# Kernel tuning notes

Measured on AMD Instinct MI355X. Metric: run time of the kernel, lower is better.

Reference implementation:

```python
import jax, jax.numpy as jnp
import numpy as np

DIM = 64
HEADS = 4
EPS_LN = 1e-6
EPS_NORM = 1e-12


def _dwconv(x, w):
    # depthwise 3x3, SAME padding; x: [B,C,H,W], w: [C,1,3,3]
    return jax.lax.conv_general_dilated(
        x, w, window_strides=(1, 1), padding='SAME',
        feature_group_count=x.shape[1],
        dimension_numbers=('NCHW', 'OIHW', 'NCHW'))


def setup_inputs() -> dict:
    key = jax.random.key(0)
    ks = jax.random.split(key, 10)
    s = 0.05
    inp = {
        'x': jax.random.normal(ks[0], (8, DIM, 256, 256), dtype=jnp.float32),
        'ln_w': jnp.ones((DIM,), jnp.float32),
        'ln_b': jnp.zeros((DIM,), jnp.float32),
        'w_q': jax.random.normal(ks[1], (DIM, DIM), jnp.float32) * s,
        'w_k': jax.random.normal(ks[2], (DIM, DIM), jnp.float32) * s,
        'w_v': jax.random.normal(ks[3], (DIM, DIM), jnp.float32) * s,
        'dw_q': jax.random.normal(ks[4], (DIM, 1, 3, 3), jnp.float32) * s,
        'dw_k': jax.random.normal(ks[5], (DIM, 1, 3, 3), jnp.float32) * s,
        'dw_v': jax.random.normal(ks[6], (DIM, 1, 3, 3), jnp.float32) * s,
        'w_proj': jax.random.normal(ks[7], (DIM, DIM, 3, 3), jnp.float32) * s,
        'w_comp': jax.random.normal(ks[8], (DIM // 4, DIM), jnp.float32) * s,
        'temperature': jnp.ones((HEADS, 1, 1), jnp.float32),
    }
    return inp


def reference(x, ln_w, ln_b, w_q, w_k, w_v, dw_q, dw_k, dw_v, w_proj, w_comp, temperature):
    b, c, h, w = x.shape
    heads = temperature.shape[0]
    hd = c // heads  # per-head channels

    # LayerNorm over channel dim (per spatial location), biased variance
    mu = jnp.mean(x, axis=1, keepdims=True)
    var = jnp.mean((x - mu) ** 2, axis=1, keepdims=True)
    xn = (x - mu) / jnp.sqrt(var + EPS_LN)
    xn = xn * ln_w[None, :, None, None] + ln_b[None, :, None, None]

    # 1x1 projections then depthwise 3x3
    q = _dwconv(jnp.einsum('oc,bchw->bohw', w_q, xn), dw_q)
    k = _dwconv(jnp.einsum('oc,bchw->bohw', w_k, xn), dw_k)
    v = _dwconv(jnp.einsum('oc,bchw->bohw', w_v, xn), dw_v)

    # [b, heads, hd, h*w]
    q = q.reshape(b, heads, hd, h * w)
    k = k.reshape(b, heads, hd, h * w)
    v = v.reshape(b, heads, hd, h * w)

    # L2 normalize along spatial axis (torch F.normalize: x / max(||x||, eps))
    q = q / jnp.maximum(jnp.linalg.norm(q, axis=-1, keepdims=True), EPS_NORM)
    k = k / jnp.maximum(jnp.linalg.norm(k, axis=-1, keepdims=True), EPS_NORM)

    # channel attention: [b, heads, hd, hd]
    attn = jnp.einsum('bhcn,bhdn->bhcd', q, k) * temperature[None]
    attn = jax.nn.softmax(attn, axis=-1)
    out = jnp.einsum('bhcd,bhdn->bhcn', attn, v).reshape(b, c, h, w)

    # 3x3 projection + residual (residual is the normalized x, per source)
    out = jax.lax.conv_general_dilated(
        out, w_proj, window_strides=(1, 1), padding='SAME',
        dimension_numbers=('NCHW', 'OIHW', 'NCHW')) + xn

    # 1x1 compress to dim//4
    return jnp.einsum('oc,bchw->bohw', w_comp, out)
```

## Files before the change

### kernel.cpp

```cpp
#include <hip/hip_runtime.h>
#include <hip/hip_bf16.h>
#include <stdint.h>

#define BB 8
#define CC 64
#define HH 256
#define WW 256
#define NPIX 65536
#define HEADS 4
#define HD 16
#define PRS 76

using bf16 = __hip_bfloat16;
typedef __attribute__((ext_vector_type(8))) short short8;
typedef __attribute__((ext_vector_type(4))) float f32x4;

__device__ __forceinline__ float bf2f(bf16 v) { return __bfloat162float(v); }
__device__ __forceinline__ bf16 f2bf(float v) { return __float2bfloat16(v); }
__device__ __forceinline__ short f2bfs(float f) { bf16 h = __float2bfloat16(f); return *reinterpret_cast<short*>(&h); }
__device__ __forceinline__ float bfs2f(short s) { return __uint_as_float(((uint32_t)(uint16_t)s) << 16); }
__device__ __forceinline__ uint32_t pk2(float a, float b) {
  return (uint32_t)(uint16_t)f2bfs(a) | ((uint32_t)(uint16_t)f2bfs(b) << 16);
}
__device__ __forceinline__ short8 zero8() { short8 z = {0, 0, 0, 0, 0, 0, 0, 0}; return z; }

__device__ __forceinline__ void load8bf(const bf16* p, float* o) {
  uint4 u = *reinterpret_cast<const uint4*>(p);
  o[0] = __uint_as_float(u.x << 16);
  o[1] = __uint_as_float(u.x & 0xffff0000u);
  o[2] = __uint_as_float(u.y << 16);
  o[3] = __uint_as_float(u.y & 0xffff0000u);
  o[4] = __uint_as_float(u.z << 16);
  o[5] = __uint_as_float(u.z & 0xffff0000u);
  o[6] = __uint_as_float(u.w << 16);
  o[7] = __uint_as_float(u.w & 0xffff0000u);
}

__global__ void k_prep(const float* __restrict__ w_comp, const float* __restrict__ w_proj,
                       const float* __restrict__ w_q, const float* __restrict__ w_k,
                       const float* __restrict__ w_v,
                       short* __restrict__ wcpb, short* __restrict__ wqkvb,
                       short* __restrict__ wcb) {
  int idx = blockIdx.x * 256 + threadIdx.x;
  if (idx < 9 * 16 * 64) {
    int c = idx & 63;
    int o = (idx >> 6) & 15;
    int kk = idx >> 10;
    float acc = 0.f;
    for (int m = 0; m < 64; ++m)
      acc += w_comp[o * 64 + m] * w_proj[(m * 64 + c) * 9 + kk];
    wcpb[idx] = f2bfs(acc);
  }
  if (idx < 3 * 4096) {
    const float* Ws[3] = {w_q, w_k, w_v};
    wqkvb[idx] = f2bfs(Ws[idx >> 12][idx & 4095]);
  }
  if (idx < 1024) wcb[idx] = f2bfs(w_comp[idx]);
}

__global__ __launch_bounds__(256)
void k_ln(const float* __restrict__ x, const float* __restrict__ ln_w,
          const float* __restrict__ ln_b, short* __restrict__ xnb) {
  const int tid = threadIdx.x;
  const int b = blockIdx.x >> 8;
  const int n = ((blockIdx.x & 255) << 8) + tid;
  const float* xp = x + (size_t)b * CC * NPIX + n;
  float v[64];
  float s = 0.f, s2 = 0.f;
#pragma unroll
  for (int c = 0; c < 64; ++c) {
    float t0 = xp[(size_t)c * NPIX];
    v[c] = t0; s += t0; s2 += t0 * t0;
  }
  const float mu = s * (1.f / 64.f);
  const float r = rsqrtf(s2 * (1.f / 64.f) - mu * mu + 1e-6f);
  short* op = xnb + ((size_t)b * NPIX + n) * 64;
#pragma unroll
  for (int c8 = 0; c8 < 8; ++c8) {
    uint32_t pk[4];
#pragma unroll
    for (int j = 0; j < 4; ++j) {
      const int c0 = c8 * 8 + 2 * j;
      float f0 = (v[c0] - mu) * r * ln_w[c0] + ln_b[c0];
      float f1 = (v[c0 + 1] - mu) * r * ln_w[c0 + 1] + ln_b[c0 + 1];
      pk[j] = pk2(f0, f1);
    }
    *reinterpret_cast<uint4*>(op + c8 * 8) = make_uint4(pk[0], pk[1], pk[2], pk[3]);
  }
}

__global__ __launch_bounds__(512)
void k_qkv(const short* __restrict__ xnb, const short* __restrict__ wqkvb,
           const short* __restrict__ wcb,
           const float* __restrict__ dw_q, const float* __restrict__ dw_k,
           const float* __restrict__ dw_v,
           bf16* __restrict__ qo, bf16* __restrict__ ko,
           short* __restrict__ aov, short* __restrict__ res16) {
  __shared__ short pr_s[336 * PRS];
  const int tid = threadIdx.x;
  const int lane = tid & 63;
  const int wv = tid >> 6;
  const int olocal = lane & 15;
  const int g = lane >> 4;
  const int t = blockIdx.y;
  const int tx = blockIdx.x & 15, ty = (blockIdx.x >> 4) & 15, b = blockIdx.x >> 8;
  const int x0 = tx * 16 - 1, y0 = ty * 16 - 1;

  if (t == 0) {
    short8 wc0 = *reinterpret_cast<const short8*>(wcb + olocal * 64 + g * 8);
    short8 wc1 = *reinterpret_cast<const short8*>(wcb + olocal * 64 + 32 + g * 8);
#pragma unroll
    for (int t2 = 0; t2 < 2; ++t2) {
      const int oy = wv * 2 + t2;
      const int n = (ty * 16 + oy) * WW + tx * 16 + olocal;
      const short* bb = xnb + ((size_t)b * NPIX + n) * 64 + g * 8;
      short8 b0 = *reinterpret_cast<const short8*>(bb);
      short8 b1 = *reinterpret_cast<const short8*>(bb + 32);
      f32x4 acc = {0.f, 0.f, 0.f, 0.f};
      acc = __builtin_amdgcn_mfma_f32_16x16x32_bf16(wc0, b0, acc, 0, 0, 0);
      acc = __builtin_amdgcn_mfma_f32_16x16x32_bf16(wc1, b1, acc, 0, 0, 0);
      uint2 st;
      st.x = pk2(acc[0], acc[1]);
      st.y = pk2(acc[2], acc[3]);
      *reinterpret_cast<uint2*>(&res16[((size_t)b * NPIX + n) * 16 + g * 4]) = st;
    }
  }

  short8 Bt[4][2];
#pragma unroll
  for (int ot = 0; ot < 4; ++ot) {
    const short* wb = wqkvb + t * 4096 + (ot * 16 + olocal) * 64 + g * 8;
    Bt[ot][0] = *reinterpret_cast<const short8*>(wb);
    Bt[ot][1] = *reinterpret_cast<const short8*>(wb + 32);
  }

  short8 a0[3], a1[3];
#pragma unroll
  for (int j = 0; j < 3; ++j) {
    const int pt = wv + j * 8;
    const int p = pt * 16 + olocal;
    const int py = y0 + p / 18;
    const int px_ = x0 + p % 18;
    const bool vld = (pt < 21) && (p < 324) && ((unsigned)py < 256u) && ((unsigned)px_ < 256u);
    if (vld) {
      const short* ab = xnb + ((size_t)b * NPIX + py * WW + px_) * 64 + g * 8;
      a0[j] = *reinterpret_cast<const short8*>(ab);
      a1[j] = *reinterpret_cast<const short8*>(ab + 32);
    } else {
      a0[j] = zero8();
      a1[j] = zero8();
    }
  }
#pragma unroll
  for (int j = 0; j < 3; ++j) {
    const int pt = wv + j * 8;
    if (pt >= 21) continue;
#pragma unroll
    for (int ot = 0; ot < 4; ++ot) {
      f32x4 acc = {0.f, 0.f, 0.f, 0.f};
      acc = __builtin_amdgcn_mfma_f32_16x16x32_bf16(a0[j], Bt[ot][0], acc, 0, 0, 0);
      acc = __builtin_amdgcn_mfma_f32_16x16x32_bf16(a1[j], Bt[ot][1], acc, 0, 0, 0);
#pragma unroll
      for (int r = 0; r < 4; ++r)
        pr_s[(pt * 16 + g * 4 + r) * PRS + ot * 16 + olocal] = f2bfs(acc[r]);
    }
  }
  __syncthreads();

  const float* dmt = (t == 0) ? dw_q : (t == 1) ? dw_k : dw_v;
  float dmr[8][9];
#pragma unroll
  for (int u = 0; u < 8; ++u)
#pragma unroll
    for (int kk = 0; kk < 9; ++kk)
      dmr[u][kk] = dmt[(wv * 8 + u) * 9 + kk];
  bf16* ob = ((t == 0) ? qo : ko) + (size_t)b * CC * NPIX;
#pragma unroll
  for (int i = 0; i < 4; ++i) {
    const int pxl = lane + i * 64;
    const int oy = pxl >> 4, ox = pxl & 15;
    float acc8[8] = {0.f, 0.f, 0.f, 0.f, 0.f, 0.f, 0.f, 0.f};
#pragma unroll
    for (int ky = 0; ky < 3; ++ky)
#pragma unroll
      for (int kx = 0; kx < 3; ++kx) {
        const short8 pv = *reinterpret_cast<const short8*>(
            &pr_s[((oy + ky) * 18 + ox + kx) * PRS + wv * 8]);
        const int kk = ky * 3 + kx;
#pragma unroll
        for (int u = 0; u < 8; ++u)
          acc8[u] += dmr[u][kk] * bfs2f(pv[u]);
      }
    const int n = (ty * 16 + oy) * WW + tx * 16 + ox;
    if (t < 2) {
#pragma unroll
      for (int u = 0; u < 8; ++u)
        ob[(size_t)(wv * 8 + u) * NPIX + n] = f2bf(acc8[u]);
    } else {
      uint4 st = make_uint4(pk2(acc8[0], acc8[1]), pk2(acc8[2], acc8[3]),
                            pk2(acc8[4], acc8[5]), pk2(acc8[6], acc8[7]));
      *reinterpret_cast<uint4*>(&aov[((size_t)b * NPIX + n) * 64 + wv * 8]) = st;
    }
  }
}

__global__ __launch_bounds__(256)
void k_logits(const bf16* __restrict__ q, const bf16* __restrict__ kk_,
              float* __restrict__ Spart, float* __restrict__ Qpart,
              float* __restrict__ Kpart) {
  const int tid = threadIdx.x;
  const int lane = tid & 63;
  const int wv = tid >> 6;
  const int bh = blockIdx.x >> 6;
  const int chunk = blockIdx.x & 63;
  const int row = lane & 15;
  const int g = lane >> 4;
  const short* qp = (const short*)q + (size_t)(bh * HD + row) * NPIX;
  const short* kp = (const short*)kk_ + (size_t)(bh * HD + row) * NPIX;
  const int n0 = chunk * 1024 + wv * 256 + g * 8;
  f32x4 s = {0.f, 0.f, 0.f, 0.f};
  f32x4 sq = {0.f, 0.f, 0.f, 0.f};
  f32x4 sk = {0.f, 0.f, 0.f, 0.f};
#pragma unroll
  for (int it = 0; it < 8; ++it) {
    const int n = n0 + it * 32;
    short8 qa = *reinterpret_cast<const short8*>(qp + n);
    short8 ka = *reinterpret_cast<const short8*>(kp + n);
    s  = __builtin_amdgcn_mfma_f32_16x16x32_bf16(qa, ka, s, 0, 0, 0);
    sq = __builtin_amdgcn_mfma_f32_16x16x32_bf16(qa, qa, sq, 0, 0, 0);
    sk = __builtin_amdgcn_mfma_f32_16x16x32_bf16(ka, ka, sk, 0, 0, 0);
  }
  const size_t tile = (size_t)blockIdx.x * 4 + wv;
  float* sp = Spart + tile * 256;
#pragma unroll
  for (int r = 0; r < 4; ++r)
    sp[(g * 4 + r) * 16 + row] = s[r];
  if ((row >> 2) == g) {
    Qpart[tile * 16 + row] = sq[row & 3];
    Kpart[tile * 16 + row] = sk[row & 3];
  }
}

__global__ __launch_bounds__(256)
void k_softmax(const float* __restrict__ Spart, const float* __restrict__ Qpart,
               const float* __restrict__ Kpart, const float* __restrict__ temp,
               float* __restrict__ attn) {
  const int tid = threadIdx.x;
  const int bh = blockIdx.x;
  const int i = tid >> 4, j = tid & 15;
  float S = 0.f, qs = 0.f, ks = 0.f;
  const size_t t0 = (size_t)bh * 256;
  for (int c = 0; c < 256; ++c) {
    S += Spart[(t0 + c) * 256 + tid];
    qs += Qpart[(t0 + c) * 16 + i];
    ks += Kpart[(t0 + c) * 16 + j];
  }
  float nq = fmaxf(sqrtf(qs), 1e-12f);
  float nk = fmaxf(sqrtf(ks), 1e-12f);
  float val = S / (nq * nk) * temp[bh & 3];
  float m = val;
  for (int d = 1; d < 16; d <<= 1) m = fmaxf(m, __shfl_xor(m, d));
  float e = __expf(val - m);
  float s = e;
  for (int d = 1; d < 16; d <<= 1) s += __shfl_xor(s, d);
  attn[bh * 256 + tid] = e / s;
}

__global__ __launch_bounds__(256)
void k_attv(const float* __restrict__ attn, short* __restrict__ aov) {
  const int tid = threadIdx.x;
  const int bh = blockIdx.x >> 8;
  const int b = bh >> 2, h = bh & 3;
  const int n = ((blockIdx.x & 255) << 8) + tid;
  __shared__ float a_s[256];
  a_s[tid] = attn[bh * 256 + tid];
  __syncthreads();
  short* vp = aov + ((size_t)b * NPIX + n) * 64 + h * 16;
  float vv[16];
  load8bf((const bf16*)vp, vv);
  load8bf((const bf16*)(vp + 8), vv + 8);
  float o[16];
#pragma unroll
  for (int i = 0; i < 16; ++i) {
    float acc = 0.f;
#pragma unroll
    for (int j = 0; j < 16; ++j) acc += a_s[i * 16 + j] * vv[j];
    o[i] = acc;
  }
  uint4 lo = make_uint4(pk2(o[0], o[1]), pk2(o[2], o[3]), pk2(o[4], o[5]), pk2(o[6], o[7]));
  uint4 hi = make_uint4(pk2(o[8], o[9]), pk2(o[10], o[11]), pk2(o[12], o[13]), pk2(o[14], o[15]));
  *reinterpret_cast<uint4*>(vp) = lo;
  *reinterpret_cast<uint4*>(vp + 8) = hi;
}

__global__ __launch_bounds__(256)
void k_final(const short* __restrict__ wcpb, const short* __restrict__ ao,
             const short* __restrict__ res16, float* __restrict__ out) {
  const int tid = threadIdx.x;
  const int lane = tid & 63;
  const int wv = tid >> 6;
  const int olocal = lane & 15;
  const int g = lane >> 4;
  const int tx = blockIdx.x & 15, ty = (blockIdx.x >> 4) & 15, b = blockIdx.x >> 8;

  short8 WA[9][2];
#pragma unroll
  for (int kk = 0; kk < 9; ++kk) {
    const short* wb = wcpb + (kk * 16 + olocal) * 64 + g * 8;
    WA[kk][0] = *reinterpret_cast<const short8*>(wb);
    WA[kk][1] = *reinterpret_cast<const short8*>(wb + 32);
  }

#pragma unroll
  for (int t = 0; t < 4; ++t) {
    const int oy = wv * 4 + t;
    const int gyc = ty * 16 + oy;
    const int n0 = gyc * WW + tx * 16;
    uint2 rv = *reinterpret_cast<const uint2*>(
        &res16[((size_t)b * NPIX + n0 + olocal) * 16 + g * 4]);
    f32x4 acc;
    acc[0] = __uint_as_float(rv.x << 16);
    acc[1] = __uint_as_float(rv.x & 0xffff0000u);
    acc[2] = __uint_as_float(rv.y << 16);
    acc[3] = __uint_as_float(rv.y & 0xffff0000u);
#pragma unroll
    for (int ky = 0; ky < 3; ++ky) {
      const int gy = gyc + ky - 1;
      if ((unsigned)gy < 256u) {
#pragma unroll
        for (int kx = 0; kx < 3; ++kx) {
          const int gx = tx * 16 + kx - 1 + olocal;
          const bool vld = (unsigned)gx < 256u;
          const short* ap = ao + ((size_t)b * NPIX + gy * WW + gx) * 64 + g * 8;
          short8 b0, b1;
          if (vld) {
            b0 = *reinterpret_cast<const short8*>(ap);
            b1 = *reinterpret_cast<const short8*>(ap + 32);
          } else {
            b0 = zero8();
            b1 = zero8();
          }
          acc = __builtin_amdgcn_mfma_f32_16x16x32_bf16(WA[ky * 3 + kx][0], b0, acc, 0, 0, 0);
          acc = __builtin_amdgcn_mfma_f32_16x16x32_bf16(WA[ky * 3 + kx][1], b1, acc, 0, 0, 0);
        }
      }
    }
    float* op = out + ((size_t)b * 16 + g * 4) * NPIX + n0 + olocal;
    op[0] = acc[0];
    op[NPIX] = acc[1];
    op[2 * NPIX] = acc[2];
    op[3 * NPIX] = acc[3];
  }
}

extern "C" void kernel_launch(void* const* d_in, const int* in_sizes, int n_in,
                              void* d_out, int out_size, void* d_ws, size_t ws_size,
                              hipStream_t stream) {
  const float* x      = (const float*)d_in[0];
  const float* ln_w   = (const float*)d_in[1];
  const float* ln_b   = (const float*)d_in[2];
  const float* w_q    = (const float*)d_in[3];
  const float* w_k    = (const float*)d_in[4];
  const float* w_v    = (const float*)d_in[5];
  const float* dw_q   = (const float*)d_in[6];
  const float* dw_k   = (const float*)d_in[7];
  const float* dw_v   = (const float*)d_in[8];
  const float* w_proj = (const float*)d_in[9];
  const float* w_comp = (const float*)d_in[10];
  const float* temp   = (const float*)d_in[11];
  float* out = (float*)d_out;

  const size_t SPX = (size_t)BB * NPIX;
  short* xnb   = (short*)d_ws;
  short* qb    = xnb + SPX * 64;
  short* kb    = qb + SPX * 64;
  short* aov   = kb + SPX * 64;
  short* res16 = aov + SPX * 64;
  short* wcpb  = res16 + SPX * 16;
  short* wqkvb = wcpb + 9216;
  short* wcb   = wqkvb + 12288;
  float* Spart = (float*)(wcb + 1024);
  float* Qpart = Spart + 32 * 256 * 256;
  float* Kpart = Qpart + 32 * 256 * 16;
  float* attn  = Kpart + 32 * 256 * 16;

  k_prep<<<52, 256, 0, stream>>>(w_comp, w_proj, w_q, w_k, w_v, wcpb, wqkvb, wcb);
  k_ln<<<2048, 256, 0, stream>>>(x, ln_w, ln_b, xnb);
  dim3 gqkv(2048, 3);
  k_qkv<<<gqkv, 512, 0, stream>>>(xnb, wqkvb, wcb, dw_q, dw_k, dw_v,
                                  (bf16*)qb, (bf16*)kb, aov, res16);
  k_logits<<<2048, 256, 0, stream>>>((const bf16*)qb, (const bf16*)kb, Spart, Qpart, Kpart);
  k_softmax<<<32, 256, 0, stream>>>(Spart, Qpart, Kpart, temp, attn);
  k_attv<<<8192, 256, 0, stream>>>(attn, aov);
  k_final<<<2048, 256, 0, stream>>>(wcpb, aov, res16, out);
}
```

Measured before the change: 382.1 us.

## Fuse attention-times-V into final projection kernel via block-diagonal bf16 attention matrix

The separate k_attv pass, which read V and wrote attn·V back to global memory, is removed. Softmax now writes a block-diagonal 64x64 bf16 attention matrix per batch. The final kernel computes attn·V with MFMA for an 18x18 halo tile into shared memory, then runs the 3x3 projection from LDS instead of from global loads. The qkv kernel's MFMA operand order is also swapped so the shared-memory stores become packed 8-byte writes. The cost is recomputing attn·V on halo pixels, more LDS per block, and extra MFMA work on the zero blocks of the block-diagonal matrix.

```diff
diff --git a/kernel.cpp b/kernel.cpp
--- a/kernel.cpp
+++ b/kernel.cpp
@@ -23,18 +23,6 @@
   return (uint32_t)(uint16_t)f2bfs(a) | ((uint32_t)(uint16_t)f2bfs(b) << 16);
 }
 __device__ __forceinline__ short8 zero8() { short8 z = {0, 0, 0, 0, 0, 0, 0, 0}; return z; }
-
-__device__ __forceinline__ void load8bf(const bf16* p, float* o) {
-  uint4 u = *reinterpret_cast<const uint4*>(p);
-  o[0] = __uint_as_float(u.x << 16);
-  o[1] = __uint_as_float(u.x & 0xffff0000u);
-  o[2] = __uint_as_float(u.y << 16);
-  o[3] = __uint_as_float(u.y & 0xffff0000u);
-  o[4] = __uint_as_float(u.z << 16);
-  o[5] = __uint_as_float(u.z & 0xffff0000u);
-  o[6] = __uint_as_float(u.w << 16);
-  o[7] = __uint_as_float(u.w & 0xffff0000u);
-}
 
 __global__ void k_prep(const float* __restrict__ w_comp, const float* __restrict__ w_proj,
                        const float* __restrict__ w_q, const float* __restrict__ w_k,
@@ -155,14 +143,16 @@
   for (int j = 0; j < 3; ++j) {
     const int pt = wv + j * 8;
     if (pt >= 21) continue;
+    const int p2 = pt * 16 + olocal;
 #pragma unroll
     for (int ot = 0; ot < 4; ++ot) {
       f32x4 acc = {0.f, 0.f, 0.f, 0.f};
-      acc = __builtin_amdgcn_mfma_f32_16x16x32_bf16(a0[j], Bt[ot][0], acc, 0, 0, 0);
-      acc = __builtin_amdgcn_mfma_f32_16x16x32_bf16(a1[j], Bt[ot][1], acc, 0, 0, 0);
-#pragma unroll
-      for (int r = 0; r < 4; ++r)
-        pr_s[(pt * 16 + g * 4 + r) * PRS + ot * 16 + olocal] = f2bfs(acc[r]);
+      acc = __builtin_amdgcn_mfma_f32_16x16x32_bf16(Bt[ot][0], a0[j], acc, 0, 0, 0);
+      acc = __builtin_amdgcn_mfma_f32_16x16x32_bf16(Bt[ot][1], a1[j], acc, 0, 0, 0);
+      uint2 st;
+      st.x = pk2(acc[0], acc[1]);
+      st.y = pk2(acc[2], acc[3]);
+      *reinterpret_cast<uint2*>(&pr_s[p2 * PRS + ot * 16 + g * 4]) = st;
     }
   }
   __syncthreads();
@@ -244,9 +234,10 @@
 __global__ __launch_bounds__(256)
 void k_softmax(const float* __restrict__ Spart, const float* __restrict__ Qpart,
                const float* __restrict__ Kpart, const float* __restrict__ temp,
-               float* __restrict__ attn) {
+               short* __restrict__ attb) {
   const int tid = threadIdx.x;
   const int bh = blockIdx.x;
+  const int b = bh >> 2, h = bh & 3;
   const int i = tid >> 4, j = tid & 15;
   float S = 0.f, qs = 0.f, ks = 0.f;
   const size_t t0 = (size_t)bh * 256;
@@ -257,51 +248,70 @@
   }
   float nq = fmaxf(sqrtf(qs), 1e-12f);
   float nk = fmaxf(sqrtf(ks), 1e-12f);
-  float val = S / (nq * nk) * temp[bh & 3];
+  float val = S / (nq * nk) * temp[h];
   float m = val;
   for (int d = 1; d < 16; d <<= 1) m = fmaxf(m, __shfl_xor(m, d));
   float e = __expf(val - m);
   float s = e;
   for (int d = 1; d < 16; d <<= 1) s += __shfl_xor(s, d);
-  attn[bh * 256 + tid] = e / s;
-}
-
-__global__ __launch_bounds__(256)
-void k_attv(const float* __restrict__ attn, short* __restrict__ aov) {
-  const int tid = threadIdx.x;
-  const int bh = blockIdx.x >> 8;
-  const int b = bh >> 2, h = bh & 3;
-  const int n = ((blockIdx.x & 255) << 8) + tid;
-  __shared__ float a_s[256];
-  a_s[tid] = attn[bh * 256 + tid];
-  __syncthreads();
-  short* vp = aov + ((size_t)b * NPIX + n) * 64 + h * 16;
-  float vv[16];
-  load8bf((const bf16*)vp, vv);
-  load8bf((const bf16*)(vp + 8), vv + 8);
-  float o[16];
-#pragma unroll
-  for (int i = 0; i < 16; ++i) {
-    float acc = 0.f;
-#pragma unroll
-    for (int j = 0; j < 16; ++j) acc += a_s[i * 16 + j] * vv[j];
-    o[i] = acc;
-  }
-  uint4 lo = make_uint4(pk2(o[0], o[1]), pk2(o[2], o[3]), pk2(o[4], o[5]), pk2(o[6], o[7]));
-  uint4 hi = make_uint4(pk2(o[8], o[9]), pk2(o[10], o[11]), pk2(o[12], o[13]), pk2(o[14], o[15]));
-  *reinterpret_cast<uint4*>(vp) = lo;
-  *reinterpret_cast<uint4*>(vp + 8) = hi;
-}
-
-__global__ __launch_bounds__(256)
-void k_final(const short* __restrict__ wcpb, const short* __restrict__ ao,
-             const short* __restrict__ res16, float* __restrict__ out) {
+  attb[((size_t)b * 64 + h * 16 + i) * 64 + h * 16 + j] = f2bfs(e / s);
+#pragma unroll
+  for (int mq = 0; mq < 4; ++mq) {
+    const int idx = tid * 4 + mq;
+    const int r = idx >> 6, c = idx & 63;
+    if ((c >> 4) != h)
+      attb[((size_t)b * 64 + h * 16 + r) * 64 + c] = 0;
+  }
+}
+
+__global__ __launch_bounds__(512)
+void k_attf(const short* __restrict__ attb, const short* __restrict__ vao,
+            const short* __restrict__ wcpb, const short* __restrict__ res16,
+            float* __restrict__ out) {
+  __shared__ short ao_s[336 * PRS];
   const int tid = threadIdx.x;
   const int lane = tid & 63;
   const int wv = tid >> 6;
   const int olocal = lane & 15;
   const int g = lane >> 4;
   const int tx = blockIdx.x & 15, ty = (blockIdx.x >> 4) & 15, b = blockIdx.x >> 8;
+  const int x0 = tx * 16 - 1, y0 = ty * 16 - 1;
+
+  {
+    short8 AT[4][2];
+#pragma unroll
+    for (int ot = 0; ot < 4; ++ot) {
+      const short* ab = attb + ((size_t)b * 64 + ot * 16 + olocal) * 64 + g * 8;
+      AT[ot][0] = *reinterpret_cast<const short8*>(ab);
+      AT[ot][1] = *reinterpret_cast<const short8*>(ab + 32);
+    }
+#pragma unroll
+    for (int j = 0; j < 3; ++j) {
+      const int pt = wv + j * 8;
+      if (pt >= 21) continue;
+      const int p = pt * 16 + olocal;
+      const int py = y0 + p / 18;
+      const int px_ = x0 + p % 18;
+      const bool vld = (p < 324) && ((unsigned)py < 256u) && ((unsigned)px_ < 256u);
+      short8 b0 = zero8(), b1 = zero8();
+      if (vld) {
+        const short* vp = vao + ((size_t)b * NPIX + py * WW + px_) * 64 + g * 8;
+        b0 = *reinterpret_cast<const short8*>(vp);
+        b1 = *reinterpret_cast<const short8*>(vp + 32);
+      }
+#pragma unroll
+      for (int ot = 0; ot < 4; ++ot) {
+        f32x4 acc = {0.f, 0.f, 0.f, 0.f};
+        acc = __builtin_amdgcn_mfma_f32_16x16x32_bf16(AT[ot][0], b0, acc, 0, 0, 0);
+        acc = __builtin_amdgcn_mfma_f32_16x16x32_bf16(AT[ot][1], b1, acc, 0, 0, 0);
+        uint2 st;
+        st.x = pk2(acc[0], acc[1]);
+        st.y = pk2(acc[2], acc[3]);
+        *reinterpret_cast<uint2*>(&ao_s[p * PRS + ot * 16 + g * 4]) = st;
+      }
+    }
+  }
+  __syncthreads();
 
   short8 WA[9][2];
 #pragma unroll
@@ -310,12 +320,10 @@
     WA[kk][0] = *reinterpret_cast<const short8*>(wb);
     WA[kk][1] = *reinterpret_cast<const short8*>(wb + 32);
   }
-
-#pragma unroll
-  for (int t = 0; t < 4; ++t) {
-    const int oy = wv * 4 + t;
-    const int gyc = ty * 16 + oy;
-    const int n0 = gyc * WW + tx * 16;
+#pragma unroll
+  for (int s = 0; s < 2; ++s) {
+    const int oy = wv * 2 + s;
+    const int n0 = (ty * 16 + oy) * WW + tx * 16;
     uint2 rv = *reinterpret_cast<const uint2*>(
         &res16[((size_t)b * NPIX + n0 + olocal) * 16 + g * 4]);
     f32x4 acc;
@@ -324,27 +332,15 @@
     acc[2] = __uint_as_float(rv.y << 16);
     acc[3] = __uint_as_float(rv.y & 0xffff0000u);
 #pragma unroll
-    for (int ky = 0; ky < 3; ++ky) {
-      const int gy = gyc + ky - 1;
-      if ((unsigned)gy < 256u) {
-#pragma unroll
-        for (int kx = 0; kx < 3; ++kx) {
-          const int gx = tx * 16 + kx - 1 + olocal;
-          const bool vld = (unsigned)gx < 256u;
-          const short* ap = ao + ((size_t)b * NPIX + gy * WW + gx) * 64 + g * 8;
-          short8 b0, b1;
-          if (vld) {
-            b0 = *reinterpret_cast<const short8*>(ap);
-            b1 = *reinterpret_cast<const short8*>(ap + 32);
-          } else {
-            b0 = zero8();
-            b1 = zero8();
-          }
-          acc = __builtin_amdgcn_mfma_f32_16x16x32_bf16(WA[ky * 3 + kx][0], b0, acc, 0, 0, 0);
-          acc = __builtin_amdgcn_mfma_f32_16x16x32_bf16(WA[ky * 3 + kx][1], b1, acc, 0, 0, 0);
-        }
+    for (int ky = 0; ky < 3; ++ky)
+#pragma unroll
+      for (int kx = 0; kx < 3; ++kx) {
+        const int hp = (oy + ky) * 18 + olocal + kx;
+        short8 b0 = *reinterpret_cast<const short8*>(&ao_s[hp * PRS + g * 8]);
+        short8 b1 = *reinterpret_cast<const short8*>(&ao_s[hp * PRS + 32 + g * 8]);
+        acc = __builtin_amdgcn_mfma_f32_16x16x32_bf16(WA[ky * 3 + kx][0], b0, acc, 0, 0, 0);
+        acc = __builtin_amdgcn_mfma_f32_16x16x32_bf16(WA[ky * 3 + kx][1], b1, acc, 0, 0, 0);
       }
-    }
     float* op = out + ((size_t)b * 16 + g * 4) * NPIX + n0 + olocal;
     op[0] = acc[0];
     op[NPIX] = acc[1];
@@ -379,10 +375,10 @@
   short* wcpb  = res16 + SPX * 16;
   short* wqkvb = wcpb + 9216;
   short* wcb   = wqkvb + 12288;
-  float* Spart = (float*)(wcb + 1024);
+  short* attb  = wcb + 1024;
+  float* Spart = (float*)(attb + 8 * 64 * 64 + 512);
   float* Qpart = Spart + 32 * 256 * 256;
   float* Kpart = Qpart + 32 * 256 * 16;
-  float* attn  = Kpart + 32 * 256 * 16;
 
   k_prep<<<52, 256, 0, stream>>>(w_comp, w_proj, w_q, w_k, w_v, wcpb, wqkvb, wcb);
   k_ln<<<2048, 256, 0, stream>>>(x, ln_w, ln_b, xnb);
@@ -390,7 +386,6 @@
   k_qkv<<<gqkv, 512, 0, stream>>>(xnb, wqkvb, wcb, dw_q, dw_k, dw_v,
                                   (bf16*)qb, (bf16*)kb, aov, res16);
   k_logits<<<2048, 256, 0, stream>>>((const bf16*)qb, (const bf16*)kb, Spart, Qpart, Kpart);
-  k_softmax<<<32, 256, 0, stream>>>(Spart, Qpart, Kpart, temp, attn);
-  k_attv<<<8192, 256, 0, stream>>>(attn, aov);
-  k_final<<<2048, 256, 0, stream>>>(wcpb, aov, res16, out);
-}
+  k_softmax<<<32, 256, 0, stream>>>(Spart, Qpart, Kpart, temp, attb);
+  k_attf<<<2048, 512, 0, stream>>>(attb, aov, wcpb, res16, out);
+}
```

After: 320.6 us. -16.1%, faster.
